# Kernel tuning notes

Measured on AMD Instinct MI355X. Metric: run time of the kernel, lower is better.

Reference implementation:

```python
import jax, jax.numpy as jnp
import numpy as np


def setup_inputs() -> dict:
    key = jax.random.key(0)
    k1, k2 = jax.random.split(key)
    B, S, D = 16, 2048, 128
    x1 = jax.random.normal(k1, (B, S, D), dtype=jnp.float32)
    x2 = jax.random.normal(k2, (B, S, D), dtype=jnp.float32)
    return {"x1": x1, "x2": x2}


def reference(x1, x2):
    # Mutual cross attention (eval mode, dropout is identity).
    d = x1.shape[-1]
    scale = 1.0 / jnp.sqrt(jnp.asarray(d, dtype=x1.dtype))
    # scores[b,i,j] = <x1[b,i], x2[b,j]> / sqrt(d). The second score matrix in the
    # original (key @ query^T) is exactly the transpose, so compute once.
    scores = jnp.einsum("bid,bjd->bij", x1, x2) * scale  # [B,S,S]
    out_A = jnp.einsum("bij,bjd->bid", jax.nn.softmax(scores, axis=-1), x2)
    # softmax over rows of scores^T == softmax over axis -2 of scores, then transpose
    out_B = jnp.einsum("bij,bid->bjd", jax.nn.softmax(scores, axis=-2), x1)
    return out_A + out_B
```

## Files before the change

kernel.cpp:

```cpp
#include <hip/hip_runtime.h>

typedef _Float16 f16;
typedef f16 f16x8 __attribute__((ext_vector_type(8)));
typedef f16 f16x4 __attribute__((ext_vector_type(4)));
typedef float f32x4 __attribute__((ext_vector_type(4)));

#define MFMA_F16(a, b, c) __builtin_amdgcn_mfma_f32_16x16x32_f16((a), (b), (c), 0, 0, 0)

namespace {
constexpr int SN = 2048;
constexpr int DN = 128;
constexpr int KVB = 64;
constexpr int NW = 4;
constexpr int QW = 16;
constexpr int QB = NW * QW;
constexpr float SCALE = 0.08838834764831845f;
}

__device__ __forceinline__ int kidx(int kv, int d)  { return kv * DN  + (d  ^ ((kv & 7) << 3)); }
__device__ __forceinline__ int vidx(int d, int kv)  { return d  * KVB + (kv ^ (((d ^ (d >> 3)) & 7) << 3)); }
__device__ __forceinline__ int pidx(int q, int kv)  { return q  * KVB + (kv ^ ((q  & 7) << 3)); }

__global__ __launch_bounds__(256, 2)
void mca_kernel(const float* __restrict__ x1, const float* __restrict__ x2,
                float* __restrict__ out)
{
    __shared__ __align__(16) f16 sK[KVB * DN];
    __shared__ __align__(16) f16 sV[DN * KVB];
    __shared__ __align__(16) f16 sP[NW * QW * KVB];

    const int b  = blockIdx.x >> 5;
    const int q0 = (blockIdx.x & 31) * QB;
    const int t  = threadIdx.x;
    const int w  = t >> 6;
    const int l  = t & 63;
    const int lg = l >> 4;
    const int ll = l & 15;

    const int rg = t >> 4;
    const int cg = t & 15;

    f16* sPw = sP + w * (QW * KVB);

    f32x4 oSum[8];
    #pragma unroll
    for (int n = 0; n < 8; ++n) oSum[n] = (f32x4){0.f, 0.f, 0.f, 0.f};

    for (int pass = 0; pass < 2; ++pass) {
        const float* xq  = pass ? x2 : x1;
        const float* xkv = pass ? x1 : x2;
        const float* qb  = xq  + ((size_t)b * SN + q0 + w * QW) * DN;
        const float* kb  = xkv + (size_t)b * SN * DN;

        f16x8 qf[4];
        #pragma unroll
        for (int kk = 0; kk < 4; ++kk) {
            const float* p = qb + ll * DN + kk * 32 + lg * 8;
            float4 a0 = *(const float4*)p;
            float4 a1 = *(const float4*)(p + 4);
            f16x8 q;
            q[0] = (f16)(a0.x * SCALE); q[1] = (f16)(a0.y * SCALE);
            q[2] = (f16)(a0.z * SCALE); q[3] = (f16)(a0.w * SCALE);
            q[4] = (f16)(a1.x * SCALE); q[5] = (f16)(a1.y * SCALE);
            q[6] = (f16)(a1.z * SCALE); q[7] = (f16)(a1.w * SCALE);
            qf[kk] = q;
        }

        f32x4 oAcc[8];
        #pragma unroll
        for (int n = 0; n < 8; ++n) oAcc[n] = (f32x4){0.f, 0.f, 0.f, 0.f};
        float mrun = -1e30f;
        float lrun = 0.f;

        for (int kv0 = 0; kv0 < SN; kv0 += KVB) {
            __syncthreads();
            {
                const float* src = kb + (size_t)kv0 * DN;
                float hv[4][8];
                #pragma unroll
                for (int rr = 0; rr < 4; ++rr) {
                    const float* p = src + (4 * rg + rr) * DN + 8 * cg;
                    float4 a0 = *(const float4*)p;
                    float4 a1 = *(const float4*)(p + 4);
                    hv[rr][0] = a0.x; hv[rr][1] = a0.y; hv[rr][2] = a0.z; hv[rr][3] = a0.w;
                    hv[rr][4] = a1.x; hv[rr][5] = a1.y; hv[rr][6] = a1.z; hv[rr][7] = a1.w;
                }
                #pragma unroll
                for (int rr = 0; rr < 4; ++rr) {
                    f16x8 kp;
                    #pragma unroll
                    for (int j = 0; j < 8; ++j) kp[j] = (f16)hv[rr][j];
                    *(f16x8*)&sK[kidx(4 * rg + rr, 8 * cg)] = kp;
                }
                #pragma unroll
                for (int i = 0; i < 8; ++i) {
                    f16x4 vp;
                    #pragma unroll
                    for (int rr = 0; rr < 4; ++rr) vp[rr] = (f16)hv[rr][i];
                    *(f16x4*)&sV[vidx(8 * cg + i, 4 * rg)] = vp;
                }
            }
            __syncthreads();

            f32x4 sacc[4];
            #pragma unroll
            for (int mt = 0; mt < 4; ++mt) sacc[mt] = (f32x4){0.f, 0.f, 0.f, 0.f};
            #pragma unroll
            for (int kk = 0; kk < 4; ++kk) {
                #pragma unroll
                for (int mt = 0; mt < 4; ++mt) {
                    f16x8 ka = *(const f16x8*)&sK[kidx(mt * 16 + ll, kk * 32 + lg * 8)];
                    sacc[mt] = MFMA_F16(ka, qf[kk], sacc[mt]);
                }
            }

            {
                float tm = sacc[0][0];
                #pragma unroll
                for (int mt = 0; mt < 4; ++mt)
                    #pragma unroll
                    for (int r = 0; r < 4; ++r) tm = fmaxf(tm, sacc[mt][r]);
                tm = fmaxf(tm, __shfl_xor(tm, 16));
                tm = fmaxf(tm, __shfl_xor(tm, 32));
                float mnew = fmaxf(mrun, tm);
                float corr = __expf(mrun - mnew);
                float ps = 0.f;
                #pragma unroll
                for (int mt = 0; mt < 4; ++mt) {
                    f16x4 pk;
                    #pragma unroll
                    for (int r = 0; r < 4; ++r) {
                        float pv = __expf(sacc[mt][r] - mnew);
                        ps += pv;
                        pk[r] = (f16)pv;
                    }
                    *(f16x4*)&sPw[pidx(ll, mt * 16 + 4 * lg)] = pk;
                }
                ps += __shfl_xor(ps, 16);
                ps += __shfl_xor(ps, 32);
                lrun = lrun * corr + ps;
                mrun = mnew;
                #pragma unroll
                for (int r = 0; r < 4; ++r) {
                    float c2 = __shfl(corr, 4 * lg + r);
                    #pragma unroll
                    for (int nd = 0; nd < 8; ++nd) oAcc[nd][r] *= c2;
                }
            }

            f16x8 pa[2];
            #pragma unroll
            for (int kc = 0; kc < 2; ++kc)
                pa[kc] = *(const f16x8*)&sPw[pidx(ll, kc * 32 + lg * 8)];
            #pragma unroll
            for (int nd = 0; nd < 8; ++nd) {
                #pragma unroll
                for (int kc = 0; kc < 2; ++kc) {
                    f16x8 vb = *(const f16x8*)&sV[vidx(nd * 16 + ll, kc * 32 + lg * 8)];
                    oAcc[nd] = MFMA_F16(pa[kc], vb, oAcc[nd]);
                }
            }
        }

        #pragma unroll
        for (int r = 0; r < 4; ++r) {
            float li = __shfl(lrun, 4 * lg + r);
            float inv = 1.0f / li;
            #pragma unroll
            for (int nd = 0; nd < 8; ++nd) oSum[nd][r] += oAcc[nd][r] * inv;
        }
    }

    float* ob = out + ((size_t)b * SN + q0 + w * QW) * DN;
    #pragma unroll
    for (int r = 0; r < 4; ++r) {
        const int row = 4 * lg + r;
        #pragma unroll
        for (int nd = 0; nd < 8; ++nd)
            ob[row * DN + nd * 16 + ll] = oSum[nd][r];
    }
}

extern "C" void kernel_launch(void* const* d_in, const int* in_sizes, int n_in,
                              void* d_out, int out_size, void* d_ws, size_t ws_size,
                              hipStream_t stream) {
    const float* x1 = (const float*)d_in[0];
    const float* x2 = (const float*)d_in[1];
    float* out = (float*)d_out;
    const int B = in_sizes[0] / (SN * DN);
    dim3 grid(B * (SN / QB));
    dim3 block(256);
    hipLaunchKernelGGL(mca_kernel, grid, block, 0, stream, x1, x2, out);
}
```

Measured before the change: 149.7 us.

## Split mutual-attention passes across blocks and combine with atomic adds

Each block now handles a single attention direction instead of looping over both, doubling the grid and relying on atomicAdd into a zeroed output to sum the two results. Block indices are remapped so that neighbouring launches spread across batches and directions, launch bounds request higher occupancy, and the softmax uses exp2 with log2(e) folded into the query scale. The intent is to fill more compute units and shorten the per-block critical path. The cost is an extra memset, atomic writes, and an index mapping hardcoded to batch size 16.

```diff
diff --git a/kernel.cpp b/kernel.cpp
--- a/kernel.cpp
+++ b/kernel.cpp
@@ -14,14 +14,14 @@
 constexpr int NW = 4;
 constexpr int QW = 16;
 constexpr int QB = NW * QW;
-constexpr float SCALE = 0.08838834764831845f;
+constexpr float SCALE_L2E = 0.1275213897f;
 }
 
 __device__ __forceinline__ int kidx(int kv, int d)  { return kv * DN  + (d  ^ ((kv & 7) << 3)); }
 __device__ __forceinline__ int vidx(int d, int kv)  { return d  * KVB + (kv ^ (((d ^ (d >> 3)) & 7) << 3)); }
 __device__ __forceinline__ int pidx(int q, int kv)  { return q  * KVB + (kv ^ ((q  & 7) << 3)); }
 
-__global__ __launch_bounds__(256, 2)
+__global__ __launch_bounds__(256, 4)
 void mca_kernel(const float* __restrict__ x1, const float* __restrict__ x2,
                 float* __restrict__ out)
 {
@@ -29,8 +29,12 @@
     __shared__ __align__(16) f16 sV[DN * KVB];
     __shared__ __align__(16) f16 sP[NW * QW * KVB];
 
-    const int b  = blockIdx.x >> 5;
-    const int q0 = (blockIdx.x & 31) * QB;
+    const int gid  = blockIdx.x;
+    const int work = (gid & 7) * 128 + (gid >> 3);
+    const int pass = work >> 9;
+    const int b    = (work >> 5) & 15;
+    const int q0   = (work & 31) * QB;
+
     const int t  = threadIdx.x;
     const int w  = t >> 6;
     const int l  = t & 63;
@@ -42,142 +46,130 @@
 
     f16* sPw = sP + w * (QW * KVB);
 
-    f32x4 oSum[8];
+    const float* xq  = pass ? x2 : x1;
+    const float* xkv = pass ? x1 : x2;
+    const float* qb  = xq  + ((size_t)b * SN + q0 + w * QW) * DN;
+    const float* kb  = xkv + (size_t)b * SN * DN;
+
+    f16x8 qf[4];
     #pragma unroll
-    for (int n = 0; n < 8; ++n) oSum[n] = (f32x4){0.f, 0.f, 0.f, 0.f};
+    for (int kk = 0; kk < 4; ++kk) {
+        const float* p = qb + ll * DN + kk * 32 + lg * 8;
+        float4 a0 = *(const float4*)p;
+        float4 a1 = *(const float4*)(p + 4);
+        f16x8 q;
+        q[0] = (f16)(a0.x * SCALE_L2E); q[1] = (f16)(a0.y * SCALE_L2E);
+        q[2] = (f16)(a0.z * SCALE_L2E); q[3] = (f16)(a0.w * SCALE_L2E);
+        q[4] = (f16)(a1.x * SCALE_L2E); q[5] = (f16)(a1.y * SCALE_L2E);
+        q[6] = (f16)(a1.z * SCALE_L2E); q[7] = (f16)(a1.w * SCALE_L2E);
+        qf[kk] = q;
+    }
 
-    for (int pass = 0; pass < 2; ++pass) {
-        const float* xq  = pass ? x2 : x1;
-        const float* xkv = pass ? x1 : x2;
-        const float* qb  = xq  + ((size_t)b * SN + q0 + w * QW) * DN;
-        const float* kb  = xkv + (size_t)b * SN * DN;
+    f32x4 oAcc[8];
+    #pragma unroll
+    for (int n = 0; n < 8; ++n) oAcc[n] = (f32x4){0.f, 0.f, 0.f, 0.f};
+    float mrun = -1e30f;
+    float lrun = 0.f;
 
-        f16x8 qf[4];
+    for (int kv0 = 0; kv0 < SN; kv0 += KVB) {
+        __syncthreads();
+        {
+            const float* src = kb + (size_t)kv0 * DN;
+            float hv[4][8];
+            #pragma unroll
+            for (int rr = 0; rr < 4; ++rr) {
+                const float* p = src + (4 * rg + rr) * DN + 8 * cg;
+                float4 a0 = *(const float4*)p;
+                float4 a1 = *(const float4*)(p + 4);
+                hv[rr][0] = a0.x; hv[rr][1] = a0.y; hv[rr][2] = a0.z; hv[rr][3] = a0.w;
+                hv[rr][4] = a1.x; hv[rr][5] = a1.y; hv[rr][6] = a1.z; hv[rr][7] = a1.w;
+            }
+            #pragma unroll
+            for (int rr = 0; rr < 4; ++rr) {
+                f16x8 kp;
+                #pragma unroll
+                for (int j = 0; j < 8; ++j) kp[j] = (f16)hv[rr][j];
+                *(f16x8*)&sK[kidx(4 * rg + rr, 8 * cg)] = kp;
+            }
+            #pragma unroll
+            for (int i = 0; i < 8; ++i) {
+                f16x4 vp;
+                #pragma unroll
+                for (int rr = 0; rr < 4; ++rr) vp[rr] = (f16)hv[rr][i];
+                *(f16x4*)&sV[vidx(8 * cg + i, 4 * rg)] = vp;
+            }
+        }
+        __syncthreads();
+
+        f32x4 sacc[4];
+        #pragma unroll
+        for (int mt = 0; mt < 4; ++mt) sacc[mt] = (f32x4){0.f, 0.f, 0.f, 0.f};
         #pragma unroll
         for (int kk = 0; kk < 4; ++kk) {
-            const float* p = qb + ll * DN + kk * 32 + lg * 8;
-            float4 a0 = *(const float4*)p;
-            float4 a1 = *(const float4*)(p + 4);
-            f16x8 q;
-            q[0] = (f16)(a0.x * SCALE); q[1] = (f16)(a0.y * SCALE);
-            q[2] = (f16)(a0.z * SCALE); q[3] = (f16)(a0.w * SCALE);
-            q[4] = (f16)(a1.x * SCALE); q[5] = (f16)(a1.y * SCALE);
-            q[6] = (f16)(a1.z * SCALE); q[7] = (f16)(a1.w * SCALE);
-            qf[kk] = q;
-        }
-
-        f32x4 oAcc[8];
-        #pragma unroll
-        for (int n = 0; n < 8; ++n) oAcc[n] = (f32x4){0.f, 0.f, 0.f, 0.f};
-        float mrun = -1e30f;
-        float lrun = 0.f;
-
-        for (int kv0 = 0; kv0 < SN; kv0 += KVB) {
-            __syncthreads();
-            {
-                const float* src = kb + (size_t)kv0 * DN;
-                float hv[4][8];
-                #pragma unroll
-                for (int rr = 0; rr < 4; ++rr) {
-                    const float* p = src + (4 * rg + rr) * DN + 8 * cg;
-                    float4 a0 = *(const float4*)p;
-                    float4 a1 = *(const float4*)(p + 4);
-                    hv[rr][0] = a0.x; hv[rr][1] = a0.y; hv[rr][2] = a0.z; hv[rr][3] = a0.w;
-                    hv[rr][4] = a1.x; hv[rr][5] = a1.y; hv[rr][6] = a1.z; hv[rr][7] = a1.w;
-                }
-                #pragma unroll
-                for (int rr = 0; rr < 4; ++rr) {
-                    f16x8 kp;
-                    #pragma unroll
-                    for (int j = 0; j < 8; ++j) kp[j] = (f16)hv[rr][j];
-                    *(f16x8*)&sK[kidx(4 * rg + rr, 8 * cg)] = kp;
-                }
-                #pragma unroll
-                for (int i = 0; i < 8; ++i) {
-                    f16x4 vp;
-                    #pragma unroll
-                    for (int rr = 0; rr < 4; ++rr) vp[rr] = (f16)hv[rr][i];
-                    *(f16x4*)&sV[vidx(8 * cg + i, 4 * rg)] = vp;
-                }
-            }
-            __syncthreads();
-
-            f32x4 sacc[4];
             #pragma unroll
-            for (int mt = 0; mt < 4; ++mt) sacc[mt] = (f32x4){0.f, 0.f, 0.f, 0.f};
-            #pragma unroll
-            for (int kk = 0; kk < 4; ++kk) {
-                #pragma unroll
-                for (int mt = 0; mt < 4; ++mt) {
-                    f16x8 ka = *(const f16x8*)&sK[kidx(mt * 16 + ll, kk * 32 + lg * 8)];
-                    sacc[mt] = MFMA_F16(ka, qf[kk], sacc[mt]);
-                }
-            }
-
-            {
-                float tm = sacc[0][0];
-                #pragma unroll
-                for (int mt = 0; mt < 4; ++mt)
-                    #pragma unroll
-                    for (int r = 0; r < 4; ++r) tm = fmaxf(tm, sacc[mt][r]);
-                tm = fmaxf(tm, __shfl_xor(tm, 16));
-                tm = fmaxf(tm, __shfl_xor(tm, 32));
-                float mnew = fmaxf(mrun, tm);
-                float corr = __expf(mrun - mnew);
-                float ps = 0.f;
-                #pragma unroll
-                for (int mt = 0; mt < 4; ++mt) {
-                    f16x4 pk;
-                    #pragma unroll
-                    for (int r = 0; r < 4; ++r) {
-                        float pv = __expf(sacc[mt][r] - mnew);
-                        ps += pv;
-                        pk[r] = (f16)pv;
-                    }
-                    *(f16x4*)&sPw[pidx(ll, mt * 16 + 4 * lg)] = pk;
-                }
-                ps += __shfl_xor(ps, 16);
-                ps += __shfl_xor(ps, 32);
-                lrun = lrun * corr + ps;
-                mrun = mnew;
-                #pragma unroll
-                for (int r = 0; r < 4; ++r) {
-                    float c2 = __shfl(corr, 4 * lg + r);
-                    #pragma unroll
-                    for (int nd = 0; nd < 8; ++nd) oAcc[nd][r] *= c2;
-                }
-            }
-
-            f16x8 pa[2];
-            #pragma unroll
-            for (int kc = 0; kc < 2; ++kc)
-                pa[kc] = *(const f16x8*)&sPw[pidx(ll, kc * 32 + lg * 8)];
-            #pragma unroll
-            for (int nd = 0; nd < 8; ++nd) {
-                #pragma unroll
-                for (int kc = 0; kc < 2; ++kc) {
-                    f16x8 vb = *(const f16x8*)&sV[vidx(nd * 16 + ll, kc * 32 + lg * 8)];
-                    oAcc[nd] = MFMA_F16(pa[kc], vb, oAcc[nd]);
-                }
+            for (int mt = 0; mt < 4; ++mt) {
+                f16x8 ka = *(const f16x8*)&sK[kidx(mt * 16 + ll, kk * 32 + lg * 8)];
+                sacc[mt] = MFMA_F16(ka, qf[kk], sacc[mt]);
             }
         }
 
+        {
+            float tm = sacc[0][0];
+            #pragma unroll
+            for (int mt = 0; mt < 4; ++mt)
+                #pragma unroll
+                for (int r = 0; r < 4; ++r) tm = fmaxf(tm, sacc[mt][r]);
+            tm = fmaxf(tm, __shfl_xor(tm, 16));
+            tm = fmaxf(tm, __shfl_xor(tm, 32));
+            float mnew = fmaxf(mrun, tm);
+            float corr = exp2f(mrun - mnew);
+            float ps = 0.f;
+            #pragma unroll
+            for (int mt = 0; mt < 4; ++mt) {
+                f16x4 pk;
+                #pragma unroll
+                for (int r = 0; r < 4; ++r) {
+                    float pv = exp2f(sacc[mt][r] - mnew);
+                    ps += pv;
+                    pk[r] = (f16)pv;
+                }
+                *(f16x4*)&sPw[pidx(ll, mt * 16 + 4 * lg)] = pk;
+            }
+            ps += __shfl_xor(ps, 16);
+            ps += __shfl_xor(ps, 32);
+            lrun = lrun * corr + ps;
+            mrun = mnew;
+            #pragma unroll
+            for (int r = 0; r < 4; ++r) {
+                float c2 = __shfl(corr, 4 * lg + r);
+                #pragma unroll
+                for (int nd = 0; nd < 8; ++nd) oAcc[nd][r] *= c2;
+            }
+        }
+
+        f16x8 pa[2];
         #pragma unroll
-        for (int r = 0; r < 4; ++r) {
-            float li = __shfl(lrun, 4 * lg + r);
-            float inv = 1.0f / li;
+        for (int kc = 0; kc < 2; ++kc)
+            pa[kc] = *(const f16x8*)&sPw[pidx(ll, kc * 32 + lg * 8)];
+        #pragma unroll
+        for (int nd = 0; nd < 8; ++nd) {
             #pragma unroll
-            for (int nd = 0; nd < 8; ++nd) oSum[nd][r] += oAcc[nd][r] * inv;
+            for (int kc = 0; kc < 2; ++kc) {
+                f16x8 vb = *(const f16x8*)&sV[vidx(nd * 16 + ll, kc * 32 + lg * 8)];
+                oAcc[nd] = MFMA_F16(pa[kc], vb, oAcc[nd]);
+            }
         }
     }
 
     float* ob = out + ((size_t)b * SN + q0 + w * QW) * DN;
     #pragma unroll
     for (int r = 0; r < 4; ++r) {
+        float li = __shfl(lrun, 4 * lg + r);
+        float inv = 1.0f / li;
         const int row = 4 * lg + r;
         #pragma unroll
         for (int nd = 0; nd < 8; ++nd)
-            ob[row * DN + nd * 16 + ll] = oSum[nd][r];
+            atomicAdd(&ob[row * DN + nd * 16 + ll], oAcc[nd][r] * inv);
     }
 }
 
@@ -188,7 +180,8 @@
     const float* x2 = (const float*)d_in[1];
     float* out = (float*)d_out;
     const int B = in_sizes[0] / (SN * DN);
-    dim3 grid(B * (SN / QB));
+    hipMemsetAsync(d_out, 0, (size_t)out_size * sizeof(float), stream);
+    dim3 grid(2 * B * (SN / QB));
     dim3 block(256);
     hipLaunchKernelGGL(mca_kernel, grid, block, 0, stream, x1, x2, out);
 }
```

Result: slower. 154.4 us (+3.1%).
